# Kernel optimization log

Hardware: AMD Instinct MI355X
Metric: run time of the kernel (lower is better)

The kernel has to match this reference:

```python
import jax, jax.numpy as jnp
import numpy as np

TAU = 2.0        # LIFNode default tau
V_TH = 1.0       # v_threshold
BN_EPS = 1e-5


def setup_inputs() -> dict:
    key = jax.random.key(0)
    k1, k2 = jax.random.split(key)
    T, B, C, V, E = 16, 512, 2, 25, 256
    x = jax.random.normal(k1, (T, B, C, V), dtype=jnp.float32)
    W = jax.random.normal(k2, (E, C), dtype=jnp.float32) * 0.5  # conv1x1 weight [out,in]
    gamma = jnp.ones((E,), dtype=jnp.float32)
    beta = jnp.zeros((E,), dtype=jnp.float32)
    return {"x": x, "W": W, "gamma": gamma, "beta": beta}


def reference(x, W, gamma, beta):
    # x: [T, B, C, V]; conv1d(k=1) == channel-mixing matmul
    y = jnp.einsum('tbcv,ec->tbev', x, W)  # [T, B, E, V]
    # BatchNorm1d in training mode: stats over (T*B, V) per channel
    mean = jnp.mean(y, axis=(0, 1, 3), keepdims=True)
    var = jnp.var(y, axis=(0, 1, 3), keepdims=True)
    y = (y - mean) * jax.lax.rsqrt(var + BN_EPS)
    y = y * gamma[None, None, :, None] + beta[None, None, :, None]
    # Multi-step LIF: v += (x - (v - v_reset))/tau; spike = v >= v_th; hard reset to v_reset=0
    v0 = jnp.zeros(y.shape[1:], dtype=y.dtype)  # [B, E, V]
    def step(v, xt):
        v = v + (xt - v) / TAU
        spike = (v >= V_TH).astype(v.dtype)
        v = v * (1.0 - spike)  # hard reset, v_reset = 0
        return v, spike
    _, spikes = jax.lax.scan(step, v0, y)
    return spikes  # [T, B, E, V]
```

## Files before the change

### kernel.cpp

```cpp
#include <hip/hip_runtime.h>
#include <math.h>

constexpr int T = 16, B = 512, C = 2, V = 25, E = 256;
constexpr int EV  = E * V;
constexpr int BEV = B * EV;
constexpr int XT  = B * C * V;
constexpr int NB  = 1600;
constexpr int CHUNKS = 25;
constexpr int BPC = 64;
constexpr int NROWS = 7;
constexpr float NF = 204800.0f;

typedef float f32x4 __attribute__((ext_vector_type(4)));

#define WS_M32(ws) ((float*)(ws))
#define WS_R32(ws) ((float*)(ws) + E)

template<int PASS>
__global__ void __launch_bounds__(256) k_bs(const float* __restrict__ x,
                                            const float* __restrict__ W,
                                            const float* __restrict__ ws,
                                            float* __restrict__ bs) {
    __shared__ float sx[NROWS * 50];
    int p  = blockIdx.x;
    int q0 = p * 128;
    int row_lo = q0 / 25;
    for (int i = threadIdx.x; i < NROWS * 50; i += 256) {
        int r = i / 50;
        if (row_lo + r < 8192) sx[i] = x[(row_lo + r) * 50 + (i - r * 50)];
    }
    __syncthreads();

    int e = threadIdx.x;
    float w0 = W[e * 2 + 0];
    float w1 = W[e * 2 + 1];
    float mn = (PASS == 1) ? WS_M32(ws)[e] : 0.0f;

    int v   = q0 - row_lo * 25;
    int off = v;
    float r[8];
    #pragma unroll
    for (int k = 0; k < 128; k++) {
        float y = __fadd_rn(__fmul_rn(w0, sx[off]), __fmul_rn(w1, sx[off + 25]));
        if (PASS == 1) {
            float d = __fsub_rn(y, mn);
            y = __fmul_rn(d, d);
        }
        int j = k & 7;
        r[j] = (k < 8) ? y : __fadd_rn(r[j], y);
        v++; off++;
        if (v == 25) { v = 0; off += 25; }
    }
    bs[p * 256 + e] =
        __fadd_rn(__fadd_rn(__fadd_rn(r[0], r[1]), __fadd_rn(r[2], r[3])),
                  __fadd_rn(__fadd_rn(r[4], r[5]), __fadd_rn(r[6], r[7])));
}

template<int WHICH>
__global__ void __launch_bounds__(256) k_comb(const float* __restrict__ bs,
                                              float* __restrict__ ws) {
    __shared__ float cb[NB];
    __shared__ float csum[CHUNKS];
    int e = blockIdx.x;
    for (int i = threadIdx.x; i < NB; i += 256) cb[i] = bs[i * 256 + e];
    __syncthreads();
    if (threadIdx.x < CHUNKS) {
        int c = threadIdx.x;
        float t[BPC];
        #pragma unroll
        for (int i = 0; i < BPC; i++) t[i] = cb[c * BPC + i];
        #pragma unroll
        for (int m = BPC / 2; m >= 1; m >>= 1) {
            #pragma unroll
            for (int i = 0; i < m; i++)
                t[i] = __fadd_rn(t[2 * i], t[2 * i + 1]);
        }
        csum[c] = t[0];
    }
    __syncthreads();
    if (threadIdx.x == 0) {
        float acc = 0.0f;
        #pragma unroll
        for (int c = 0; c < CHUNKS; c++) acc = __fadd_rn(acc, csum[c]);
        if (WHICH == 0) {
            WS_M32(ws)[e] = __fdiv_rn(acc, NF);
        } else {
            float var = __fdiv_rn(acc, NF);
            WS_R32(ws)[e] = __fdiv_rn(1.0f, __fsqrt_rn(__fadd_rn(var, 1e-5f)));
        }
    }
}

__global__ void __launch_bounds__(256) k_main(const float* __restrict__ x,
                                              const float* __restrict__ W,
                                              const float* __restrict__ g,
                                              const float* __restrict__ bta,
                                              const float* __restrict__ ws,
                                              float* __restrict__ out) {
    __shared__ float sx[2 * T * 50];
    int blk = blockIdx.x;
    int gi0 = blk * 1024;
    int b0  = gi0 / EV;
    int nb  = ((gi0 + 1023) / EV == b0) ? 1 : 2;
    for (int i = threadIdx.x; i < nb * 800; i += 256) {
        int bi  = i / 800;
        int r   = i - bi * 800;
        int tt  = r / 50;
        sx[i] = x[(b0 + bi) * 50 + tt * XT + (r - tt * 50)];
    }
    __syncthreads();

    int gi  = gi0 + threadIdx.x * 4;
    int b   = gi / EV;
    int rem = gi - b * EV;
    int e0  = rem / V;
    int v0  = rem - e0 * V;
    int sb  = (b - b0) * 800;
    int e1  = (e0 < E - 1) ? e0 + 1 : e0;
    float w00 = W[e0 * 2], w01 = W[e0 * 2 + 1];
    float w10 = W[e1 * 2], w11 = W[e1 * 2 + 1];
    float mn0 = WS_M32(ws)[e0], mn1 = WS_M32(ws)[e1];
    float rs0 = WS_R32(ws)[e0], rs1 = WS_R32(ws)[e1];
    float ga0 = g[e0],  ga1 = g[e1];
    float be0 = bta[e0], be1 = bta[e1];

    float wA[4], wB[4], mn[4], rs[4], ga[4], be[4];
    int   vv[4];
    #pragma unroll
    for (int j = 0; j < 4; j++) {
        int  vj = v0 + j;
        bool cr = (vj >= V);
        vv[j] = cr ? vj - V : vj;
        wA[j] = cr ? w10 : w00;  wB[j] = cr ? w11 : w01;
        mn[j] = cr ? mn1 : mn0;  rs[j] = cr ? rs1 : rs0;
        ga[j] = cr ? ga1 : ga0;  be[j] = cr ? be1 : be0;
    }

    float vm[4] = {0.0f, 0.0f, 0.0f, 0.0f};
    #pragma unroll
    for (int t = 0; t < T; t++) {
        f32x4 o;
        #pragma unroll
        for (int j = 0; j < 4; j++) {
            float x0 = sx[sb + t * 50 + vv[j]];
            float x1 = sx[sb + t * 50 + 25 + vv[j]];
            float y = __fadd_rn(__fmul_rn(wA[j], x0), __fmul_rn(wB[j], x1));
            y = __fmul_rn(__fsub_rn(y, mn[j]), rs[j]);
            y = __fadd_rn(__fmul_rn(y, ga[j]), be[j]);
            float d = __fmul_rn(__fsub_rn(y, vm[j]), 0.5f);
            vm[j] = __fadd_rn(vm[j], d);
            bool sp = (vm[j] >= 1.0f);
            o[j] = sp ? 1.0f : 0.0f;
            if (sp) vm[j] = 0.0f;
        }
        __builtin_nontemporal_store(o,
            reinterpret_cast<f32x4*>(&out[(size_t)t * BEV + gi]));
    }
}

extern "C" void kernel_launch(void* const* d_in, const int* in_sizes, int n_in,
                              void* d_out, int out_size, void* d_ws, size_t ws_size,
                              hipStream_t stream) {
    (void)in_sizes; (void)n_in; (void)out_size; (void)ws_size;
    const float* x  = (const float*)d_in[0];
    const float* W  = (const float*)d_in[1];
    const float* g  = (const float*)d_in[2];
    const float* bb = (const float*)d_in[3];
    float* ws = (float*)d_ws;
    float* bs = (float*)d_out;

    k_bs<0><<<NB, 256, 0, stream>>>(x, W, ws, bs);
    k_comb<0><<<E, 256, 0, stream>>>(bs, ws);
    k_bs<1><<<NB, 256, 0, stream>>>(x, W, ws, bs);
    k_comb<1><<<E, 256, 0, stream>>>(bs, ws);
    k_main<<<BEV / 1024, 256, 0, stream>>>(x, W, g, bb, ws, (float*)d_out);
}
```

Before: 259.8 us.

## Fuse five launches into one cooperative kernel with grid syncs

```diff
diff --git a/kernel.cpp b/kernel.cpp
--- a/kernel.cpp
+++ b/kernel.cpp
@@ -1,5 +1,8 @@
 #include <hip/hip_runtime.h>
+#include <hip/hip_cooperative_groups.h>
 #include <math.h>
+
+namespace cg = cooperative_groups;
 
 constexpr int T = 16, B = 512, C = 2, V = 25, E = 256;
 constexpr int EV  = E * V;
@@ -10,6 +13,7 @@
 constexpr int BPC = 64;
 constexpr int NROWS = 7;
 constexpr float NF = 204800.0f;
+constexpr int GRID = 512, TPB = 256;
 
 typedef float f32x4 __attribute__((ext_vector_type(4)));
 
@@ -17,145 +21,183 @@
 #define WS_R32(ws) ((float*)(ws) + E)
 
 template<int PASS>
-__global__ void __launch_bounds__(256) k_bs(const float* __restrict__ x,
-                                            const float* __restrict__ W,
-                                            const float* __restrict__ ws,
-                                            float* __restrict__ bs) {
-    __shared__ float sx[NROWS * 50];
-    int p  = blockIdx.x;
-    int q0 = p * 128;
-    int row_lo = q0 / 25;
-    for (int i = threadIdx.x; i < NROWS * 50; i += 256) {
-        int r = i / 50;
-        if (row_lo + r < 8192) sx[i] = x[(row_lo + r) * 50 + (i - r * 50)];
+__device__ __forceinline__ void phase_bs(const float* __restrict__ x,
+                                         const float* __restrict__ W,
+                                         const float* __restrict__ ws,
+                                         float* __restrict__ bs,
+                                         float* __restrict__ sm) {
+    #pragma unroll 1
+    for (int rd = 0; rd < (NB + GRID - 1) / GRID; rd++) {
+        int pb = rd * GRID + blockIdx.x;
+        bool act = (pb < NB);
+        int q0 = pb * 128;
+        int row_lo = q0 / 25;
+        if (act) {
+            for (int i = threadIdx.x; i < NROWS * 50; i += TPB) {
+                int r = i / 50;
+                if (row_lo + r < 8192) sm[i] = x[(row_lo + r) * 50 + (i - r * 50)];
+            }
+        }
+        __syncthreads();
+        if (act) {
+            int e = threadIdx.x;
+            float w0 = W[e * 2 + 0];
+            float w1 = W[e * 2 + 1];
+            float mn = (PASS == 1) ? WS_M32(ws)[e] : 0.0f;
+            int v   = q0 - row_lo * 25;
+            int off = v;
+            float rg[8];
+            #pragma unroll
+            for (int k = 0; k < 128; k++) {
+                float y = __fadd_rn(__fmul_rn(w0, sm[off]), __fmul_rn(w1, sm[off + 25]));
+                if (PASS == 1) {
+                    float d = __fsub_rn(y, mn);
+                    y = __fmul_rn(d, d);
+                }
+                int j = k & 7;
+                rg[j] = (k < 8) ? y : __fadd_rn(rg[j], y);
+                v++; off++;
+                if (v == 25) { v = 0; off += 25; }
+            }
+            bs[pb * 256 + e] =
+                __fadd_rn(__fadd_rn(__fadd_rn(rg[0], rg[1]), __fadd_rn(rg[2], rg[3])),
+                          __fadd_rn(__fadd_rn(rg[4], rg[5]), __fadd_rn(rg[6], rg[7])));
+        }
+        __syncthreads();
     }
-    __syncthreads();
-
-    int e = threadIdx.x;
-    float w0 = W[e * 2 + 0];
-    float w1 = W[e * 2 + 1];
-    float mn = (PASS == 1) ? WS_M32(ws)[e] : 0.0f;
-
-    int v   = q0 - row_lo * 25;
-    int off = v;
-    float r[8];
-    #pragma unroll
-    for (int k = 0; k < 128; k++) {
-        float y = __fadd_rn(__fmul_rn(w0, sx[off]), __fmul_rn(w1, sx[off + 25]));
-        if (PASS == 1) {
-            float d = __fsub_rn(y, mn);
-            y = __fmul_rn(d, d);
-        }
-        int j = k & 7;
-        r[j] = (k < 8) ? y : __fadd_rn(r[j], y);
-        v++; off++;
-        if (v == 25) { v = 0; off += 25; }
+}
+
+template<int WHICH>
+__device__ __forceinline__ void phase_comb(const float* __restrict__ bs,
+                                           float* __restrict__ ws,
+                                           float* __restrict__ sm) {
+    int e = blockIdx.x;
+    if (e < E) {
+        float* cb   = sm;
+        float* csum = sm + NB;
+        for (int i = threadIdx.x; i < NB; i += TPB) cb[i] = bs[i * 256 + e];
+        __syncthreads();
+        if (threadIdx.x < CHUNKS) {
+            int c = threadIdx.x;
+            float t[BPC];
+            #pragma unroll
+            for (int i = 0; i < BPC; i++) t[i] = cb[c * BPC + i];
+            #pragma unroll
+            for (int m = BPC / 2; m >= 1; m >>= 1) {
+                #pragma unroll
+                for (int i = 0; i < m; i++)
+                    t[i] = __fadd_rn(t[2 * i], t[2 * i + 1]);
+            }
+            csum[c] = t[0];
+        }
+        __syncthreads();
+        if (threadIdx.x == 0) {
+            float acc = 0.0f;
+            #pragma unroll
+            for (int c = 0; c < CHUNKS; c++) acc = __fadd_rn(acc, csum[c]);
+            if (WHICH == 0) {
+                WS_M32(ws)[e] = __fdiv_rn(acc, NF);
+            } else {
+                float var = __fdiv_rn(acc, NF);
+                WS_R32(ws)[e] = __fdiv_rn(1.0f, __fsqrt_rn(__fadd_rn(var, 1e-5f)));
+            }
+        }
+        __syncthreads();
     }
-    bs[p * 256 + e] =
-        __fadd_rn(__fadd_rn(__fadd_rn(r[0], r[1]), __fadd_rn(r[2], r[3])),
-                  __fadd_rn(__fadd_rn(r[4], r[5]), __fadd_rn(r[6], r[7])));
-}
-
-template<int WHICH>
-__global__ void __launch_bounds__(256) k_comb(const float* __restrict__ bs,
-                                              float* __restrict__ ws) {
-    __shared__ float cb[NB];
-    __shared__ float csum[CHUNKS];
-    int e = blockIdx.x;
-    for (int i = threadIdx.x; i < NB; i += 256) cb[i] = bs[i * 256 + e];
-    __syncthreads();
-    if (threadIdx.x < CHUNKS) {
-        int c = threadIdx.x;
-        float t[BPC];
-        #pragma unroll
-        for (int i = 0; i < BPC; i++) t[i] = cb[c * BPC + i];
-        #pragma unroll
-        for (int m = BPC / 2; m >= 1; m >>= 1) {
-            #pragma unroll
-            for (int i = 0; i < m; i++)
-                t[i] = __fadd_rn(t[2 * i], t[2 * i + 1]);
-        }
-        csum[c] = t[0];
+}
+
+__device__ __forceinline__ void phase_main(const float* __restrict__ x,
+                                           const float* __restrict__ W,
+                                           const float* __restrict__ g,
+                                           const float* __restrict__ bta,
+                                           const float* __restrict__ ws,
+                                           float* __restrict__ out,
+                                           float* __restrict__ sm) {
+    #pragma unroll 1
+    for (int rd = 0; rd < (3200 + GRID - 1) / GRID; rd++) {
+        int blk = rd * GRID + blockIdx.x;
+        bool act = (blk < 3200);
+        int gi0 = blk * 1024;
+        int b0  = gi0 / EV;
+        int nb  = ((gi0 + 1023) / EV == b0) ? 1 : 2;
+        if (act) {
+            for (int i = threadIdx.x; i < nb * 800; i += TPB) {
+                int bi  = i / 800;
+                int r   = i - bi * 800;
+                int tt  = r / 50;
+                sm[i] = x[(b0 + bi) * 50 + tt * XT + (r - tt * 50)];
+            }
+        }
+        __syncthreads();
+        if (act) {
+            int gi  = gi0 + threadIdx.x * 4;
+            int b   = gi / EV;
+            int rem = gi - b * EV;
+            int e0  = rem / V;
+            int v0  = rem - e0 * V;
+            int sb  = (b - b0) * 800;
+            int e1  = (e0 < E - 1) ? e0 + 1 : e0;
+            float w00 = W[e0 * 2], w01 = W[e0 * 2 + 1];
+            float w10 = W[e1 * 2], w11 = W[e1 * 2 + 1];
+            float mn0 = WS_M32(ws)[e0], mn1 = WS_M32(ws)[e1];
+            float rs0 = WS_R32(ws)[e0], rs1 = WS_R32(ws)[e1];
+            float ga0 = g[e0],  ga1 = g[e1];
+            float be0 = bta[e0], be1 = bta[e1];
+
+            float wA[4], wB[4], mn[4], rs[4], ga[4], be[4];
+            int   vv[4];
+            #pragma unroll
+            for (int j = 0; j < 4; j++) {
+                int  vj = v0 + j;
+                bool cr = (vj >= V);
+                vv[j] = cr ? vj - V : vj;
+                wA[j] = cr ? w10 : w00;  wB[j] = cr ? w11 : w01;
+                mn[j] = cr ? mn1 : mn0;  rs[j] = cr ? rs1 : rs0;
+                ga[j] = cr ? ga1 : ga0;  be[j] = cr ? be1 : be0;
+            }
+
+            float vm[4] = {0.0f, 0.0f, 0.0f, 0.0f};
+            #pragma unroll
+            for (int t = 0; t < T; t++) {
+                f32x4 o;
+                #pragma unroll
+                for (int j = 0; j < 4; j++) {
+                    float x0 = sm[sb + t * 50 + vv[j]];
+                    float x1 = sm[sb + t * 50 + 25 + vv[j]];
+                    float y = __fadd_rn(__fmul_rn(wA[j], x0), __fmul_rn(wB[j], x1));
+                    y = __fmul_rn(__fsub_rn(y, mn[j]), rs[j]);
+                    y = __fadd_rn(__fmul_rn(y, ga[j]), be[j]);
+                    float d = __fmul_rn(__fsub_rn(y, vm[j]), 0.5f);
+                    vm[j] = __fadd_rn(vm[j], d);
+                    bool sp = (vm[j] >= 1.0f);
+                    o[j] = sp ? 1.0f : 0.0f;
+                    if (sp) vm[j] = 0.0f;
+                }
+                __builtin_nontemporal_store(o,
+                    reinterpret_cast<f32x4*>(&out[(size_t)t * BEV + gi]));
+            }
+        }
+        __syncthreads();
     }
-    __syncthreads();
-    if (threadIdx.x == 0) {
-        float acc = 0.0f;
-        #pragma unroll
-        for (int c = 0; c < CHUNKS; c++) acc = __fadd_rn(acc, csum[c]);
-        if (WHICH == 0) {
-            WS_M32(ws)[e] = __fdiv_rn(acc, NF);
-        } else {
-            float var = __fdiv_rn(acc, NF);
-            WS_R32(ws)[e] = __fdiv_rn(1.0f, __fsqrt_rn(__fadd_rn(var, 1e-5f)));
-        }
-    }
-}
-
-__global__ void __launch_bounds__(256) k_main(const float* __restrict__ x,
-                                              const float* __restrict__ W,
-                                              const float* __restrict__ g,
-                                              const float* __restrict__ bta,
-                                              const float* __restrict__ ws,
-                                              float* __restrict__ out) {
-    __shared__ float sx[2 * T * 50];
-    int blk = blockIdx.x;
-    int gi0 = blk * 1024;
-    int b0  = gi0 / EV;
-    int nb  = ((gi0 + 1023) / EV == b0) ? 1 : 2;
-    for (int i = threadIdx.x; i < nb * 800; i += 256) {
-        int bi  = i / 800;
-        int r   = i - bi * 800;
-        int tt  = r / 50;
-        sx[i] = x[(b0 + bi) * 50 + tt * XT + (r - tt * 50)];
-    }
-    __syncthreads();
-
-    int gi  = gi0 + threadIdx.x * 4;
-    int b   = gi / EV;
-    int rem = gi - b * EV;
-    int e0  = rem / V;
-    int v0  = rem - e0 * V;
-    int sb  = (b - b0) * 800;
-    int e1  = (e0 < E - 1) ? e0 + 1 : e0;
-    float w00 = W[e0 * 2], w01 = W[e0 * 2 + 1];
-    float w10 = W[e1 * 2], w11 = W[e1 * 2 + 1];
-    float mn0 = WS_M32(ws)[e0], mn1 = WS_M32(ws)[e1];
-    float rs0 = WS_R32(ws)[e0], rs1 = WS_R32(ws)[e1];
-    float ga0 = g[e0],  ga1 = g[e1];
-    float be0 = bta[e0], be1 = bta[e1];
-
-    float wA[4], wB[4], mn[4], rs[4], ga[4], be[4];
-    int   vv[4];
-    #pragma unroll
-    for (int j = 0; j < 4; j++) {
-        int  vj = v0 + j;
-        bool cr = (vj >= V);
-        vv[j] = cr ? vj - V : vj;
-        wA[j] = cr ? w10 : w00;  wB[j] = cr ? w11 : w01;
-        mn[j] = cr ? mn1 : mn0;  rs[j] = cr ? rs1 : rs0;
-        ga[j] = cr ? ga1 : ga0;  be[j] = cr ? be1 : be0;
-    }
-
-    float vm[4] = {0.0f, 0.0f, 0.0f, 0.0f};
-    #pragma unroll
-    for (int t = 0; t < T; t++) {
-        f32x4 o;
-        #pragma unroll
-        for (int j = 0; j < 4; j++) {
-            float x0 = sx[sb + t * 50 + vv[j]];
-            float x1 = sx[sb + t * 50 + 25 + vv[j]];
-            float y = __fadd_rn(__fmul_rn(wA[j], x0), __fmul_rn(wB[j], x1));
-            y = __fmul_rn(__fsub_rn(y, mn[j]), rs[j]);
-            y = __fadd_rn(__fmul_rn(y, ga[j]), be[j]);
-            float d = __fmul_rn(__fsub_rn(y, vm[j]), 0.5f);
-            vm[j] = __fadd_rn(vm[j], d);
-            bool sp = (vm[j] >= 1.0f);
-            o[j] = sp ? 1.0f : 0.0f;
-            if (sp) vm[j] = 0.0f;
-        }
-        __builtin_nontemporal_store(o,
-            reinterpret_cast<f32x4*>(&out[(size_t)t * BEV + gi]));
-    }
+}
+
+__global__ void __launch_bounds__(TPB, 2)
+k_fused(const float* __restrict__ x, const float* __restrict__ W,
+        const float* __restrict__ g, const float* __restrict__ bta,
+        float* __restrict__ ws, float* __restrict__ out) {
+    __shared__ float sm[NB + 32];
+    cg::grid_group gr = cg::this_grid();
+    float* bs = out;
+
+    phase_bs<0>(x, W, ws, bs, sm);
+    __threadfence(); gr.sync(); __threadfence();
+    phase_comb<0>(bs, ws, sm);
+    __threadfence(); gr.sync(); __threadfence();
+    phase_bs<1>(x, W, ws, bs, sm);
+    __threadfence(); gr.sync(); __threadfence();
+    phase_comb<1>(bs, ws, sm);
+    __threadfence(); gr.sync(); __threadfence();
+    phase_main(x, W, g, bta, ws, out, sm);
 }
 
 extern "C" void kernel_launch(void* const* d_in, const int* in_sizes, int n_in,
@@ -166,12 +208,11 @@
     const float* W  = (const float*)d_in[1];
     const float* g  = (const float*)d_in[2];
     const float* bb = (const float*)d_in[3];
-    float* ws = (float*)d_ws;
-    float* bs = (float*)d_out;
-
-    k_bs<0><<<NB, 256, 0, stream>>>(x, W, ws, bs);
-    k_comb<0><<<E, 256, 0, stream>>>(bs, ws);
-    k_bs<1><<<NB, 256, 0, stream>>>(x, W, ws, bs);
-    k_comb<1><<<E, 256, 0, stream>>>(bs, ws);
-    k_main<<<BEV / 1024, 256, 0, stream>>>(x, W, g, bb, ws, (float*)d_out);
-}
+    float* ws  = (float*)d_ws;
+    float* out = (float*)d_out;
+
+    void* args[] = {(void*)&x, (void*)&W, (void*)&g, (void*)&bb,
+                    (void*)&ws, (void*)&out};
+    hipLaunchCooperativeKernel((void*)k_fused, dim3(GRID), dim3(TPB),
+                               args, 0, stream);
+}
```

Measured after the change: 724.0 us. +178.7%, slower.
